# Kernel tuning notes

Measured on AMD Instinct MI355X. Metric: run time of the kernel, lower is better.

## Reference

```python
import jax, jax.numpy as jnp
import numpy as np

B, S, H = 2, 2048, 2048
NH, NKV, HD = 16, 4, 128
GROUPS = NH // NKV  # 4
ROPE_BASE = 10000.0


def _rope_tables(seq_len, dim):
    inv_freq = 1.0 / (ROPE_BASE ** (jnp.arange(0, dim, 2, dtype=jnp.float32) / dim))
    t = jnp.arange(seq_len, dtype=jnp.float32)
    freqs = jnp.outer(t, inv_freq)            # [S, HD/2]
    emb = jnp.concatenate([freqs, freqs], -1)  # [S, HD]
    return jnp.cos(emb), jnp.sin(emb)


def _rotate_half(x):
    x1, x2 = x[..., : x.shape[-1] // 2], x[..., x.shape[-1] // 2:]
    return jnp.concatenate([-x2, x1], axis=-1)


def setup_inputs() -> dict:
    key = jax.random.key(0)
    ks = jax.random.split(key, 5)
    hidden_states = jax.random.normal(ks[0], (B, S, H), dtype=jnp.float32)
    wq = jax.random.normal(ks[1], (H, NH * HD), dtype=jnp.float32) * 0.02
    wk = jax.random.normal(ks[2], (H, NKV * HD), dtype=jnp.float32) * 0.02
    wv = jax.random.normal(ks[3], (H, NKV * HD), dtype=jnp.float32) * 0.02
    wo = jax.random.normal(ks[4], (NH * HD, H), dtype=jnp.float32) * 0.02
    # additive causal mask [1,1,S,S]
    causal = jnp.tril(jnp.ones((S, S), dtype=bool))
    attention_mask = jnp.where(causal, 0.0, jnp.finfo(jnp.float32).min)[None, None]
    return {"hidden_states": hidden_states, "attention_mask": attention_mask,
            "wq": wq, "wk": wk, "wv": wv, "wo": wo}


def reference(hidden_states, attention_mask, wq, wk, wv, wo):
    b, s, _ = hidden_states.shape
    # projections -> [B, heads, S, HD]
    q = (hidden_states @ wq).reshape(b, s, NH, HD).transpose(0, 2, 1, 3)
    k = (hidden_states @ wk).reshape(b, s, NKV, HD).transpose(0, 2, 1, 3)
    v = (hidden_states @ wv).reshape(b, s, NKV, HD).transpose(0, 2, 1, 3)
    cos, sin = _rope_tables(s, HD)             # [S, HD]
    cos = cos[None, None]; sin = sin[None, None]
    q = q * cos + _rotate_half(q) * sin
    k = k * cos + _rotate_half(k) * sin
    # GQA: repeat kv heads (matches repeat_interleave on dim=1)
    k = jnp.repeat(k, GROUPS, axis=1)
    v = jnp.repeat(v, GROUPS, axis=1)
    scores = jnp.einsum("bhqd,bhkd->bhqk", q, k) / jnp.sqrt(jnp.float32(HD))
    scores = scores + attention_mask
    probs = jax.nn.softmax(scores.astype(jnp.float32), axis=-1).astype(q.dtype)
    attn = jnp.einsum("bhqk,bhkd->bhqd", probs, v)
    attn = attn.transpose(0, 2, 1, 3).reshape(b, s, NH * HD)
    return attn @ wo
```

## Files before the change

kernel.cpp:

```cpp
#include <hip/hip_runtime.h>

typedef unsigned short u16;
typedef unsigned int u32;
typedef __attribute__((ext_vector_type(8))) __bf16 bf16x8;
typedef __attribute__((ext_vector_type(8))) u16 u16x8;
typedef __attribute__((ext_vector_type(4))) float f32x4;

#define B_ 2
#define S_ 2048
#define H_ 2048
#define NH_ 16
#define NKV_ 4
#define HD_ 128
#define QSCALE 0.1275179064f

__device__ __forceinline__ u16 f2bf(float f) {
  return __builtin_bit_cast(u16, static_cast<__bf16>(f));
}
__device__ __forceinline__ float bf2f(u16 v) {
  return __builtin_bit_cast(float, (u32)v << 16);
}
__device__ __forceinline__ void gl2lds16(const void* g, void* l) {
  __builtin_amdgcn_global_load_lds((const __attribute__((address_space(1))) u32*)g,
                                   (__attribute__((address_space(3))) u32*)l, 16, 0, 0);
}
__device__ __forceinline__ f32x4 mfma16(bf16x8 a, bf16x8 b, f32x4 c) {
  return __builtin_amdgcn_mfma_f32_16x16x32_bf16(a, b, c, 0, 0, 0);
}

__global__ __launch_bounds__(256) void cvt_f32_bf16(const float* __restrict__ in,
                                                    u16* __restrict__ out) {
  size_t i = ((size_t)blockIdx.x * 256 + threadIdx.x) * 8;
  const float4* p = (const float4*)(in + i);
  float4 a = p[0], b = p[1];
  u16x8 o;
  o[0] = f2bf(a.x); o[1] = f2bf(a.y); o[2] = f2bf(a.z); o[3] = f2bf(a.w);
  o[4] = f2bf(b.x); o[5] = f2bf(b.y); o[6] = f2bf(b.z); o[7] = f2bf(b.w);
  *(u16x8*)(out + i) = o;
}

__global__ __launch_bounds__(256) void transpose_qkv(const float* __restrict__ wq,
                                                     const float* __restrict__ wk,
                                                     const float* __restrict__ wv,
                                                     u16* __restrict__ out) {
  __shared__ float tl[32][33];
  int bx = blockIdx.x, by = blockIdx.y;
  int tx = threadIdx.x & 31, ty = threadIdx.x >> 5;
  int orow0 = bx * 32;
  const float* src;
  int scol0, C;
  if (orow0 < 2048)      { src = wq; scol0 = orow0;        C = 2048; }
  else if (orow0 < 2560) { src = wk; scol0 = orow0 - 2048; C = 512; }
  else                   { src = wv; scol0 = orow0 - 2560; C = 512; }
#pragma unroll
  for (int i = 0; i < 32; i += 8)
    tl[ty + i][tx] = src[(size_t)(by * 32 + ty + i) * C + scol0 + tx];
  __syncthreads();
#pragma unroll
  for (int i = 0; i < 32; i += 8)
    out[(size_t)(orow0 + ty + i) * 2048 + by * 32 + tx] = f2bf(tl[tx][ty + i]);
}

__global__ __launch_bounds__(256) void transpose_f32_bf16(const float* __restrict__ in,
                                                          u16* __restrict__ out,
                                                          int R, int C) {
  __shared__ float tl[32][33];
  int bx = blockIdx.x, by = blockIdx.y;
  int tx = threadIdx.x & 31, ty = threadIdx.x >> 5;
#pragma unroll
  for (int i = 0; i < 32; i += 8)
    tl[ty + i][tx] = in[(size_t)(by * 32 + ty + i) * C + bx * 32 + tx];
  __syncthreads();
#pragma unroll
  for (int i = 0; i < 32; i += 8)
    out[(size_t)(bx * 32 + ty + i) * R + by * 32 + tx] = f2bf(tl[tx][ty + i]);
}

__global__ __launch_bounds__(256) void transpose_v(const u16* __restrict__ kvb,
                                                   u16* __restrict__ vt) {
  __shared__ u16 tl[32][33];
  int sx = blockIdx.x, dx = blockIdx.y, b = blockIdx.z;
  int tx = threadIdx.x & 31, ty = threadIdx.x >> 5;
#pragma unroll
  for (int i = 0; i < 32; i += 8)
    tl[ty + i][tx] = kvb[(size_t)(b * S_ + sx * 32 + ty + i) * 1024 + 512 + dx * 32 + tx];
  __syncthreads();
#pragma unroll
  for (int i = 0; i < 32; i += 8)
    vt[(size_t)(b * 512 + dx * 32 + ty + i) * 2048 + sx * 32 + tx] = tl[tx][ty + i];
}

__global__ __launch_bounds__(256) void rope_table(float* __restrict__ tab) {
  int idx = blockIdx.x * 256 + threadIdx.x;
  int s = idx >> 6, i = idx & 63;
  float inv = exp2f((float)i * -0.20762050593045702f);
  float ang = (float)s * inv;
  tab[2 * idx] = cosf(ang);
  tab[2 * idx + 1] = sinf(ang);
}

__global__ __launch_bounds__(256) void rope_kernel(u16* __restrict__ buf,
                                                   const float* __restrict__ tab,
                                                   int rstride, int nhshift, float scale) {
  int idx = blockIdx.x * 256 + threadIdx.x;
  int grp = idx & 7;
  int h = (idx >> 3) & ((1 << nhshift) - 1);
  int tok = idx >> (3 + nhshift);
  int s = tok & (S_ - 1);
  u16* p = buf + (size_t)tok * rstride + (h << 7) + grp * 8;
  const float2* tp = (const float2*)tab + (size_t)s * 64 + grp * 8;
  u16x8 lo = *(u16x8*)p;
  u16x8 hi = *(u16x8*)(p + 64);
  u16x8 olo, ohi;
#pragma unroll
  for (int j = 0; j < 8; j++) {
    float2 cs = tp[j];
    float c = cs.x * scale, sn = cs.y * scale;
    float xl = bf2f(lo[j]), xh = bf2f(hi[j]);
    olo[j] = f2bf(xl * c - xh * sn);
    ohi[j] = f2bf(xh * c + xl * sn);
  }
  *(u16x8*)p = olo;
  *(u16x8*)(p + 64) = ohi;
}

__global__ __launch_bounds__(256) void gemm_bt1(const u16* __restrict__ A,
                                                const u16* __restrict__ BT,
                                                u16* __restrict__ Qb,
                                                u16* __restrict__ KVb,
                                                int M, int N, int K) {
  __shared__ u16 As[2 * 128 * 32];
  __shared__ u16 Bs[2 * 128 * 32];
  const int Mt = M >> 7;
  const int nwg = gridDim.x;
  int wg = (blockIdx.x & 7) * (nwg >> 3) + (blockIdx.x >> 3);
  int tm = wg % Mt, tn = wg / Mt;
  const size_t m0 = (size_t)tm << 7, n0 = (size_t)tn << 7;
  const int tid = threadIdx.x;
  const int w = tid >> 6, lane = tid & 63;
  const int g = lane >> 4, l15 = lane & 15;
  const int wr = w >> 1, wc = w & 1;

  const int r0 = tid >> 2, s0 = tid & 3;
  const int r1 = (tid + 256) >> 2, s1 = (tid + 256) & 3;
  const u16* Ar0 = A + (m0 + r0) * K + s0 * 8;
  const u16* Ar1 = A + (m0 + r1) * K + s1 * 8;
  const u16* Br0 = BT + (n0 + r0) * K + s0 * 8;
  const u16* Br1 = BT + (n0 + r1) * K + s1 * 8;

  const f32x4 Z4 = {0.f, 0.f, 0.f, 0.f};
  f32x4 acc[4][4];
#pragma unroll
  for (int m = 0; m < 4; m++)
#pragma unroll
    for (int n = 0; n < 4; n++) acc[m][n] = Z4;

  gl2lds16(Ar0, &As[w * 512]);
  gl2lds16(Ar1, &As[w * 512 + 2048]);
  gl2lds16(Br0, &Bs[w * 512]);
  gl2lds16(Br1, &Bs[w * 512 + 2048]);

  const int nk = K >> 5;
  int cur = 0;
  for (int t = 0; t < nk; ++t) {
    if (t + 1 < nk) {
      const int k0 = (t + 1) << 5;
      const int nb = (cur ^ 1) << 12;
      gl2lds16(Ar0 + k0, &As[nb + w * 512]);
      gl2lds16(Ar1 + k0, &As[nb + w * 512 + 2048]);
      gl2lds16(Br0 + k0, &Bs[nb + w * 512]);
      gl2lds16(Br1 + k0, &Bs[nb + w * 512 + 2048]);
      asm volatile("s_waitcnt vmcnt(4)" ::: "memory");
    } else {
      asm volatile("s_waitcnt vmcnt(0)" ::: "memory");
    }
    __builtin_amdgcn_sched_barrier(0);
    __builtin_amdgcn_s_barrier();
    __builtin_amdgcn_sched_barrier(0);
    const int cb = cur << 12;
    bf16x8 af[4], bfr[4];
#pragma unroll
    for (int m = 0; m < 4; m++)
      af[m] = *(const bf16x8*)&As[cb + (wr * 64 + m * 16 + l15) * 32 + g * 8];
#pragma unroll
    for (int n = 0; n < 4; n++)
      bfr[n] = *(const bf16x8*)&Bs[cb + (wc * 64 + n * 16 + l15) * 32 + g * 8];
#pragma unroll
    for (int m = 0; m < 4; m++)
#pragma unroll
      for (int n = 0; n < 4; n++) acc[m][n] = mfma16(af[m], bfr[n], acc[m][n]);
    __builtin_amdgcn_sched_barrier(0);
    __builtin_amdgcn_s_barrier();
    __builtin_amdgcn_sched_barrier(0);
    cur ^= 1;
  }

  u16* C;
  size_t cs, cbase;
  if (n0 < 2048) { C = Qb; cs = 2048; cbase = n0; }
  else           { C = KVb; cs = 1024; cbase = n0 - 2048; }
#pragma unroll
  for (int m = 0; m < 4; m++)
#pragma unroll
    for (int n = 0; n < 4; n++)
#pragma unroll
      for (int r = 0; r < 4; r++) {
        size_t row = m0 + wr * 64 + m * 16 + g * 4 + r;
        C[row * cs + cbase + wc * 64 + n * 16 + l15] = f2bf(acc[m][n][r]);
      }
}

__global__ __launch_bounds__(256) void gemm_o64(const u16* __restrict__ A,
                                                const u16* __restrict__ BT,
                                                float* __restrict__ C) {
  const int K = 2048, N = 2048;
  __shared__ u16 As[2 * 128 * 64];
  __shared__ u16 Bs[2 * 128 * 64];
  const int Mt = 32;
  const int nwg = gridDim.x;
  int wg = (blockIdx.x & 7) * (nwg >> 3) + (blockIdx.x >> 3);
  int tm = wg % Mt, tn = wg / Mt;
  const size_t m0 = (size_t)tm << 7, n0 = (size_t)tn << 7;
  const int tid = threadIdx.x;
  const int w = tid >> 6, lane = tid & 63;
  const int g = lane >> 4, l15 = lane & 15;
  const int wr = w >> 1, wc = w & 1;

  size_t aoff[4], boff[4];
#pragma unroll
  for (int ro = 0; ro < 4; ++ro) {
    int c = ro * 256 + tid;
    int row = c >> 3, seg = c & 7;
    aoff[ro] = (m0 + row) * (size_t)K + 8 * (seg ^ (row & 7));
    boff[ro] = (n0 + row) * (size_t)K + 8 * (seg ^ (row & 7));
  }

  const f32x4 Z4 = {0.f, 0.f, 0.f, 0.f};
  f32x4 acc[4][4];
#pragma unroll
  for (int m = 0; m < 4; m++)
#pragma unroll
    for (int n = 0; n < 4; n++) acc[m][n] = Z4;

#pragma unroll
  for (int ro = 0; ro < 4; ++ro) {
    gl2lds16(A + aoff[ro], &As[ro * 2048 + w * 512]);
    gl2lds16(BT + boff[ro], &Bs[ro * 2048 + w * 512]);
  }

  const int nk = K >> 6;
  int cur = 0;
  for (int t = 0; t < nk; ++t) {
    if (t + 1 < nk) {
      const int k0 = (t + 1) << 6;
      const int nb = (cur ^ 1) << 13;
#pragma unroll
      for (int ro = 0; ro < 4; ++ro) {
        gl2lds16(A + k0 + aoff[ro], &As[nb + ro * 2048 + w * 512]);
        gl2lds16(BT + k0 + boff[ro], &Bs[nb + ro * 2048 + w * 512]);
      }
      asm volatile("s_waitcnt vmcnt(8)" ::: "memory");
    } else {
      asm volatile("s_waitcnt vmcnt(0)" ::: "memory");
    }
    __builtin_amdgcn_sched_barrier(0);
    __builtin_amdgcn_s_barrier();
    __builtin_amdgcn_sched_barrier(0);
    const int cb = cur << 13;
    bf16x8 af[2][4], bfr[2][4];
#pragma unroll
    for (int kk = 0; kk < 2; ++kk) {
#pragma unroll
      for (int m = 0; m < 4; m++)
        af[kk][m] = *(const bf16x8*)&As[cb + (wr * 64 + m * 16 + l15) * 64 +
                                       ((kk * 4 + g) ^ (l15 & 7)) * 8];
#pragma unroll
      for (int n = 0; n < 4; n++)
        bfr[kk][n] = *(const bf16x8*)&Bs[cb + (wc * 64 + n * 16 + l15) * 64 +
                                        ((kk * 4 + g) ^ (l15 & 7)) * 8];
    }
#pragma unroll
    for (int kk = 0; kk < 2; ++kk)
#pragma unroll
      for (int m = 0; m < 4; m++)
#pragma unroll
        for (int n = 0; n < 4; n++)
          acc[m][n] = mfma16(af[kk][m], bfr[kk][n], acc[m][n]);
    __builtin_amdgcn_sched_barrier(0);
    __builtin_amdgcn_s_barrier();
    __builtin_amdgcn_sched_barrier(0);
    cur ^= 1;
  }

#pragma unroll
  for (int m = 0; m < 4; m++)
#pragma unroll
    for (int n = 0; n < 4; n++)
#pragma unroll
      for (int r = 0; r < 4; r++) {
        size_t row = m0 + wr * 64 + m * 16 + g * 4 + r;
        size_t col = n0 + wc * 64 + n * 16 + l15;
        C[row * (size_t)N + col] = acc[m][n][r];
      }
}

__global__ __launch_bounds__(256) void attn_kernel(const u16* __restrict__ Qb,
                                                   const u16* __restrict__ KVb,
                                                   const u16* __restrict__ Vt,
                                                   const float* __restrict__ tab,
                                                   u16* __restrict__ Ob) {
  __shared__ u16 Ks[2][64 * 128];
  __shared__ u16 Vs[2][128 * 64];
  __shared__ u16 Ps[4][16 * 72];
  const int pair = blockIdx.x, h = blockIdx.y, b = blockIdx.z;
  const int kvh = h >> 2;
  const int tid = threadIdx.x, w = tid >> 6, lane = tid & 63;
  const int g = lane >> 4, l15 = lane & 15;
  const f32x4 Z4 = {0.f, 0.f, 0.f, 0.f};
  u16x8 oneu;
#pragma unroll
  for (int j = 0; j < 8; j++) oneu[j] = 0x3f80;
  const bf16x8 ones = __builtin_bit_cast(bf16x8, oneu);

  const u16* Kbase = KVb + (size_t)b * S_ * 1024 + kvh * 128;
  const u16* Vbase = Vt + (size_t)(b * NKV_ + kvh) * HD_ * 2048;

  for (int half = 0; half < 2; ++half) {
    const int qt = half ? pair : 31 - pair;
    const int qrow0 = qt * 64 + w * 16;

    bf16x8 qf[4];
    const u16* qp = Qb + (size_t)(b * S_ + qrow0 + l15) * 2048 + h * 128;
#pragma unroll
    for (int ds = 0; ds < 4; ds++) qf[ds] = *(const bf16x8*)(qp + ds * 32 + g * 8);
    {
      const float2* tq = (const float2*)tab + (size_t)(qrow0 + l15) * 64 + g * 8;
#pragma unroll
      for (int ds = 0; ds < 2; ds++) {
        u16x8 a = __builtin_bit_cast(u16x8, qf[ds]);
        u16x8 bb = __builtin_bit_cast(u16x8, qf[ds + 2]);
#pragma unroll
        for (int j = 0; j < 8; j++) {
          float2 cs = tq[ds * 32 + j];
          float c = cs.x * QSCALE, sn = cs.y * QSCALE;
          float lo = bf2f(a[j]), hi = bf2f(bb[j]);
          a[j] = f2bf(lo * c - hi * sn);
          bb[j] = f2bf(hi * c + lo * sn);
        }
        qf[ds] = __builtin_bit_cast(bf16x8, a);
        qf[ds + 2] = __builtin_bit_cast(bf16x8, bb);
      }
    }

    float m_r[4], l_r[4];
    f32x4 oa[8];
#pragma unroll
    for (int r = 0; r < 4; r++) { m_r[r] = -1e30f; l_r[r] = 0.f; }
#pragma unroll
    for (int n = 0; n < 8; n++) oa[n] = Z4;

    const int nt = qt + 1;
#pragma unroll
    for (int ro = 0; ro < 4; ++ro) {
      int c = ro * 256 + tid;
      int kv = c >> 4, p = c & 15;
      gl2lds16(Kbase + (size_t)kv * 1024 + 8 * (p ^ (kv & 15)), &Ks[0][ro * 2048 + w * 512]);
      int d = c >> 3, p2 = c & 7;
      gl2lds16(Vbase + (size_t)d * 2048 + 8 * (p2 ^ (d & 7)), &Vs[0][ro * 2048 + w * 512]);
    }
    __syncthreads();
    int cur = 0;

    for (int t = 0; t < nt; ++t) {
      const int kv0 = t * 64;
      if (t + 1 < nt) {
        const int nkv0 = kv0 + 64;
#pragma unroll
        for (int ro = 0; ro < 4; ++ro) {
          int c = ro * 256 + tid;
          int kv = c >> 4, p = c & 15;
          gl2lds16(Kbase + (size_t)(nkv0 + kv) * 1024 + 8 * (p ^ (kv & 15)),
                   &Ks[cur ^ 1][ro * 2048 + w * 512]);
          int d = c >> 3, p2 = c & 7;
          gl2lds16(Vbase + (size_t)d * 2048 + nkv0 + 8 * (p2 ^ (d & 7)),
                   &Vs[cur ^ 1][ro * 2048 + w * 512]);
        }
      }

      f32x4 sa[4];
#pragma unroll
      for (int c16 = 0; c16 < 4; c16++) sa[c16] = Z4;
      __builtin_amdgcn_s_setprio(1);
#pragma unroll
      for (int ds = 0; ds < 4; ++ds) {
#pragma unroll
        for (int c16 = 0; c16 < 4; ++c16) {
          bf16x8 kf = *(const bf16x8*)&Ks[cur][(c16 * 16 + l15) * 128 + ((ds * 4 + g) ^ l15) * 8];
          sa[c16] = mfma16(qf[ds], kf, sa[c16]);
        }
      }
      __builtin_amdgcn_s_setprio(0);

      if (kv0 + 63 > qrow0) {
#pragma unroll
        for (int c16 = 0; c16 < 4; c16++)
#pragma unroll
          for (int r = 0; r < 4; r++) {
            if (kv0 + c16 * 16 + l15 > qrow0 + g * 4 + r) sa[c16][r] = -1e30f;
          }
      }

      float lmax[4];
#pragma unroll
      for (int r = 0; r < 4; r++)
        lmax[r] = fmaxf(fmaxf(sa[0][r], sa[1][r]), fmaxf(sa[2][r], sa[3][r]));
      bool need = (lmax[0] > m_r[0] + 11.5415603f) || (lmax[1] > m_r[1] + 11.5415603f) ||
                  (lmax[2] > m_r[2] + 11.5415603f) || (lmax[3] > m_r[3] + 11.5415603f);
      if (__any(need)) {
        float pm[4];
#pragma unroll
        for (int r = 0; r < 4; r++) pm[r] = lmax[r];
#pragma unroll
        for (int off = 1; off < 16; off <<= 1)
#pragma unroll
          for (int r = 0; r < 4; r++) pm[r] = fmaxf(pm[r], __shfl_xor(pm[r], off));
#pragma unroll
        for (int r = 0; r < 4; r++) {
          float mn = fmaxf(m_r[r], pm[r]);
          float corr = exp2f(m_r[r] - mn);
          m_r[r] = mn;
          l_r[r] *= corr;
#pragma unroll
          for (int n = 0; n < 8; n++) oa[n][r] *= corr;
        }
      }

#pragma unroll
      for (int c16 = 0; c16 < 4; c16++)
#pragma unroll
        for (int r = 0; r < 4; r++)
          Ps[w][(g * 4 + r) * 72 + c16 * 16 + l15] =
              f2bf(exp2f(sa[c16][r] - m_r[r]));
      asm volatile("s_waitcnt lgkmcnt(0)" ::: "memory");
      __builtin_amdgcn_sched_barrier(0);

      f32x4 srow = Z4;
      __builtin_amdgcn_s_setprio(1);
#pragma unroll
      for (int ks = 0; ks < 2; ++ks) {
        bf16x8 pa = *(const bf16x8*)&Ps[w][l15 * 72 + ks * 32 + g * 8];
        srow = mfma16(pa, ones, srow);
#pragma unroll
        for (int n = 0; n < 8; n++) {
          bf16x8 vf = *(const bf16x8*)&Vs[cur][(n * 16 + l15) * 64 + (((ks * 4 + g) ^ (l15 & 7))) * 8];
          oa[n] = mfma16(pa, vf, oa[n]);
        }
      }
      __builtin_amdgcn_s_setprio(0);
#pragma unroll
      for (int r = 0; r < 4; r++) l_r[r] += srow[r];

      __syncthreads();
      cur ^= 1;
    }

    float inv[4];
#pragma unroll
    for (int r = 0; r < 4; r++) inv[r] = 1.0f / l_r[r];
#pragma unroll
    for (int n = 0; n < 8; n++)
#pragma unroll
      for (int r = 0; r < 4; r++) {
        size_t row = (size_t)b * S_ + qrow0 + g * 4 + r;
        Ob[row * 2048 + h * 128 + n * 16 + l15] = f2bf(oa[n][r] * inv[r]);
      }
  }
}

extern "C" void kernel_launch(void* const* d_in, const int* in_sizes, int n_in,
                              void* d_out, int out_size, void* d_ws, size_t ws_size,
                              hipStream_t stream) {
  const float* hid = (const float*)d_in[0];
  const float* wq = (const float*)d_in[2];
  const float* wk = (const float*)d_in[3];
  const float* wv = (const float*)d_in[4];
  const float* wo = (const float*)d_in[5];
  float* out = (float*)d_out;
  char* ws = (char*)d_ws;

  u16* hb     = (u16*)(ws);
  u16* wqkvT  = (u16*)(ws + (16u << 20));
  u16* Vt     = (u16*)(ws + (16u << 20));
  float* tab  = (float*)(ws + (20u << 20));
  u16* woT    = (u16*)(ws + (20u << 20));
  u16* Qb     = (u16*)(ws + (28u << 20));
  u16* KVb    = (u16*)(ws + (44u << 20));

  cvt_f32_bf16<<<4096, 256, 0, stream>>>(hid, hb);
  transpose_qkv<<<dim3(96, 64), 256, 0, stream>>>(wq, wk, wv, wqkvT);

  gemm_bt1<<<768, 256, 0, stream>>>(hb, wqkvT, Qb, KVb, 4096, 3072, 2048);

  rope_table<<<512, 256, 0, stream>>>(tab);
  rope_kernel<<<512, 256, 0, stream>>>(KVb, tab, 1024, 2, 1.0f);

  transpose_v<<<dim3(64, 16, 2), 256, 0, stream>>>(KVb, Vt);

  attn_kernel<<<dim3(16, 16, 2), 256, 0, stream>>>(Qb, KVb, Vt, tab, hb);

  transpose_f32_bf16<<<dim3(64, 64), 256, 0, stream>>>(wo, woT, 2048, 2048);

  gemm_o64<<<512, 256, 0, stream>>>(hb, woT, out);
}
```

Before: 224.5 us.

## Fuse V transpose into QKV GEMM epilogue via LDS staging

The QKV GEMM epilogue now writes V tiles already transposed into the Vt buffer: it stages them through swizzled shared memory and emits vectorized stores. This removes the separate transpose_v kernel launch and its extra read/write pass over V. K is now stored with a row stride of 512 instead of 1024, so the rope and attention indexing change to match. The cost is an extra barrier and LDS round trip in the epilogue of the V tiles.

```diff
diff --git a/kernel.cpp b/kernel.cpp
--- a/kernel.cpp
+++ b/kernel.cpp
@@ -4,6 +4,7 @@
 typedef unsigned int u32;
 typedef __attribute__((ext_vector_type(8))) __bf16 bf16x8;
 typedef __attribute__((ext_vector_type(8))) u16 u16x8;
+typedef __attribute__((ext_vector_type(4))) u16 u16x4;
 typedef __attribute__((ext_vector_type(4))) float f32x4;
 
 #define B_ 2
@@ -76,20 +77,6 @@
     out[(size_t)(bx * 32 + ty + i) * R + by * 32 + tx] = f2bf(tl[tx][ty + i]);
 }
 
-__global__ __launch_bounds__(256) void transpose_v(const u16* __restrict__ kvb,
-                                                   u16* __restrict__ vt) {
-  __shared__ u16 tl[32][33];
-  int sx = blockIdx.x, dx = blockIdx.y, b = blockIdx.z;
-  int tx = threadIdx.x & 31, ty = threadIdx.x >> 5;
-#pragma unroll
-  for (int i = 0; i < 32; i += 8)
-    tl[ty + i][tx] = kvb[(size_t)(b * S_ + sx * 32 + ty + i) * 1024 + 512 + dx * 32 + tx];
-  __syncthreads();
-#pragma unroll
-  for (int i = 0; i < 32; i += 8)
-    vt[(size_t)(b * 512 + dx * 32 + ty + i) * 2048 + sx * 32 + tx] = tl[tx][ty + i];
-}
-
 __global__ __launch_bounds__(256) void rope_table(float* __restrict__ tab) {
   int idx = blockIdx.x * 256 + threadIdx.x;
   int s = idx >> 6, i = idx & 63;
@@ -128,9 +115,11 @@
                                                 const u16* __restrict__ BT,
                                                 u16* __restrict__ Qb,
                                                 u16* __restrict__ KVb,
+                                                u16* __restrict__ Vt,
                                                 int M, int N, int K) {
-  __shared__ u16 As[2 * 128 * 32];
-  __shared__ u16 Bs[2 * 128 * 32];
+  __shared__ u16 shm[16384];
+  u16* As = shm;
+  u16* Bs = shm + 8192;
   const int Mt = M >> 7;
   const int nwg = gridDim.x;
   int wg = (blockIdx.x & 7) * (nwg >> 3) + (blockIdx.x >> 3);
@@ -195,19 +184,49 @@
     cur ^= 1;
   }
 
-  u16* C;
-  size_t cs, cbase;
-  if (n0 < 2048) { C = Qb; cs = 2048; cbase = n0; }
-  else           { C = KVb; cs = 1024; cbase = n0 - 2048; }
-#pragma unroll
-  for (int m = 0; m < 4; m++)
-#pragma unroll
-    for (int n = 0; n < 4; n++)
-#pragma unroll
-      for (int r = 0; r < 4; r++) {
-        size_t row = m0 + wr * 64 + m * 16 + g * 4 + r;
-        C[row * cs + cbase + wc * 64 + n * 16 + l15] = f2bf(acc[m][n][r]);
-      }
+  if (n0 >= 2560) {
+#pragma unroll
+    for (int m = 0; m < 4; m++)
+#pragma unroll
+      for (int n = 0; n < 4; n++) {
+        int d_loc = wc * 64 + n * 16 + l15;
+        int slot = (wr * 16 + m * 4 + g) ^ (d_loc & 15);
+        u16x4 v;
+#pragma unroll
+        for (int r = 0; r < 4; r++) v[r] = f2bf(acc[m][n][r]);
+        *(u16x4*)&shm[d_loc * 128 + slot * 4] = v;
+      }
+    __syncthreads();
+    const int hi = tid >> 4, lo = tid & 15;
+    const size_t bb = m0 >> 11;
+    const size_t sbase = (m0 & 2047) + lo * 8;
+#pragma unroll
+    for (int c = 0; c < 8; ++c) {
+      int d_loc = c * 16 + hi;
+      int sw = d_loc & 15;
+      u16x4 va = *(const u16x4*)&shm[d_loc * 128 + ((lo * 2) ^ sw) * 4];
+      u16x4 vb = *(const u16x4*)&shm[d_loc * 128 + ((lo * 2 + 1) ^ sw) * 4];
+      u16x8 o;
+      o[0] = va[0]; o[1] = va[1]; o[2] = va[2]; o[3] = va[3];
+      o[4] = vb[0]; o[5] = vb[1]; o[6] = vb[2]; o[7] = vb[3];
+      size_t dg = (size_t)(n0 - 2560) + d_loc;
+      *(u16x8*)&Vt[(bb * 512 + dg) * 2048 + sbase] = o;
+    }
+  } else {
+    u16* C;
+    size_t cs, cbase;
+    if (n0 < 2048) { C = Qb; cs = 2048; cbase = n0; }
+    else           { C = KVb; cs = 512; cbase = n0 - 2048; }
+#pragma unroll
+    for (int m = 0; m < 4; m++)
+#pragma unroll
+      for (int n = 0; n < 4; n++)
+#pragma unroll
+        for (int r = 0; r < 4; r++) {
+          size_t row = m0 + wr * 64 + m * 16 + g * 4 + r;
+          C[row * cs + cbase + wc * 64 + n * 16 + l15] = f2bf(acc[m][n][r]);
+        }
+  }
 }
 
 __global__ __launch_bounds__(256) void gemm_o64(const u16* __restrict__ A,
@@ -322,7 +341,7 @@
   for (int j = 0; j < 8; j++) oneu[j] = 0x3f80;
   const bf16x8 ones = __builtin_bit_cast(bf16x8, oneu);
 
-  const u16* Kbase = KVb + (size_t)b * S_ * 1024 + kvh * 128;
+  const u16* Kbase = KVb + (size_t)b * S_ * 512 + kvh * 128;
   const u16* Vbase = Vt + (size_t)(b * NKV_ + kvh) * HD_ * 2048;
 
   for (int half = 0; half < 2; ++half) {
@@ -364,7 +383,7 @@
     for (int ro = 0; ro < 4; ++ro) {
       int c = ro * 256 + tid;
       int kv = c >> 4, p = c & 15;
-      gl2lds16(Kbase + (size_t)kv * 1024 + 8 * (p ^ (kv & 15)), &Ks[0][ro * 2048 + w * 512]);
+      gl2lds16(Kbase + (size_t)kv * 512 + 8 * (p ^ (kv & 15)), &Ks[0][ro * 2048 + w * 512]);
       int d = c >> 3, p2 = c & 7;
       gl2lds16(Vbase + (size_t)d * 2048 + 8 * (p2 ^ (d & 7)), &Vs[0][ro * 2048 + w * 512]);
     }
@@ -379,7 +398,7 @@
         for (int ro = 0; ro < 4; ++ro) {
           int c = ro * 256 + tid;
           int kv = c >> 4, p = c & 15;
-          gl2lds16(Kbase + (size_t)(nkv0 + kv) * 1024 + 8 * (p ^ (kv & 15)),
+          gl2lds16(Kbase + (size_t)(nkv0 + kv) * 512 + 8 * (p ^ (kv & 15)),
                    &Ks[cur ^ 1][ro * 2048 + w * 512]);
           int d = c >> 3, p2 = c & 7;
           gl2lds16(Vbase + (size_t)d * 2048 + nkv0 + 8 * (p2 ^ (d & 7)),
@@ -490,21 +509,19 @@
 
   u16* hb     = (u16*)(ws);
   u16* wqkvT  = (u16*)(ws + (16u << 20));
-  u16* Vt     = (u16*)(ws + (16u << 20));
   float* tab  = (float*)(ws + (20u << 20));
   u16* woT    = (u16*)(ws + (20u << 20));
   u16* Qb     = (u16*)(ws + (28u << 20));
   u16* KVb    = (u16*)(ws + (44u << 20));
+  u16* Vt     = (u16*)(ws + (48u << 20));
 
   cvt_f32_bf16<<<4096, 256, 0, stream>>>(hid, hb);
   transpose_qkv<<<dim3(96, 64), 256, 0, stream>>>(wq, wk, wv, wqkvT);
 
-  gemm_bt1<<<768, 256, 0, stream>>>(hb, wqkvT, Qb, KVb, 4096, 3072, 2048);
+  gemm_bt1<<<768, 256, 0, stream>>>(hb, wqkvT, Qb, KVb, Vt, 4096, 3072, 2048);
 
   rope_table<<<512, 256, 0, stream>>>(tab);
-  rope_kernel<<<512, 256, 0, stream>>>(KVb, tab, 1024, 2, 1.0f);
-
-  transpose_v<<<dim3(64, 16, 2), 256, 0, stream>>>(KVb, Vt);
+  rope_kernel<<<512, 256, 0, stream>>>(KVb, tab, 512, 2, 1.0f);
 
   attn_kernel<<<dim3(16, 16, 2), 256, 0, stream>>>(Qb, KVb, Vt, tab, hb);
 
```

Measured after the change: 224.9 us. No clear change (+0.2%).
